# Kernel optimization log

Hardware: AMD Instinct MI355X
Metric: run time of the kernel (lower is better)

Reference implementation:

```python
import jax, jax.numpy as jnp
import numpy as np
import math

N_EMBD = 1024
N_HEAD = 16
HEAD_SIZE = N_EMBD // N_HEAD
LAYER_IDX = 2
LAMBDA_INIT = 0.8 - 0.6 * math.exp(-0.3 * (LAYER_IDX - 1))
LN_EPS = 1e-5
B, T = 4, 1024


def setup_inputs() -> dict:
    key = jax.random.key(0)
    ks = jax.random.split(key, 11)
    s = 0.02  # weight init scale
    return {
        "x": jax.random.normal(ks[0], (B, T, N_EMBD), dtype=jnp.float32),
        "Wq1": jax.random.normal(ks[1], (N_EMBD, N_EMBD), dtype=jnp.float32) * s,
        "Wq2": jax.random.normal(ks[2], (N_EMBD, N_EMBD), dtype=jnp.float32) * s,
        "Wk1": jax.random.normal(ks[3], (N_EMBD, N_EMBD), dtype=jnp.float32) * s,
        "Wk2": jax.random.normal(ks[4], (N_EMBD, N_EMBD), dtype=jnp.float32) * s,
        "Wv": jax.random.normal(ks[5], (N_EMBD, 2 * N_EMBD), dtype=jnp.float32) * s,
        "Wc": jax.random.normal(ks[6], (2 * N_EMBD, N_EMBD), dtype=jnp.float32) * s,
        "lq1": jax.random.normal(ks[7], (N_HEAD, HEAD_SIZE), dtype=jnp.float32) * 0.1,
        "lk1": jax.random.normal(ks[8], (N_HEAD, HEAD_SIZE), dtype=jnp.float32) * 0.1,
        "lq2": jax.random.normal(ks[9], (N_HEAD, HEAD_SIZE), dtype=jnp.float32) * 0.1,
        "lk2": jax.random.normal(ks[10], (N_HEAD, HEAD_SIZE), dtype=jnp.float32) * 0.1,
    }


def reference(x, Wq1, Wq2, Wk1, Wk2, Wv, Wc, lq1, lk1, lq2, lk2):
    Bx, Tx, C = x.shape
    H, hs = N_HEAD, HEAD_SIZE
    scale = 1.0 / math.sqrt(hs)

    # projections -> (B, T, H, d)
    q1 = (x @ Wq1).reshape(Bx, Tx, H, hs)
    q2 = (x @ Wq2).reshape(Bx, Tx, H, hs)
    k1 = (x @ Wk1).reshape(Bx, Tx, H, hs)
    k2 = (x @ Wk2).reshape(Bx, Tx, H, hs)
    v = (x @ Wv).reshape(Bx, Tx, H, 2 * hs)

    # dual score streams (B, H, T, T)
    att1 = jnp.einsum("bqhd,bkhd->bhqk", q1, k1) * scale
    att2 = jnp.einsum("bqhd,bkhd->bhqk", q2, k2) * scale

    causal = jnp.tril(jnp.ones((Tx, Tx), dtype=bool))  # (T, T)
    neg_inf = jnp.float32(-jnp.inf)
    att1 = jnp.where(causal, att1, neg_inf)
    att2 = jnp.where(causal, att2, neg_inf)
    a1 = jax.nn.softmax(att1, axis=-1)
    a2 = jax.nn.softmax(att2, axis=-1)

    # per-head differential lambda
    lam1 = jnp.exp(jnp.sum(lq1 * lk1, axis=-1))  # (H,)
    lam2 = jnp.exp(jnp.sum(lq2 * lk2, axis=-1))  # (H,)
    lam_full = lam1 - lam2 + LAMBDA_INIT  # (H,)

    att = a1 - lam_full[None, :, None, None] * a2  # dropout = identity (eval)

    # PV matmul -> (B, T, H, 2*hs)
    y = jnp.einsum("bhqk,bkhd->bqhd", att, v)

    # subLN over last dim (no affine)
    mu = jnp.mean(y, axis=-1, keepdims=True)
    var = jnp.mean(jnp.square(y - mu), axis=-1, keepdims=True)
    y = (y - mu) / jnp.sqrt(var + LN_EPS)
    y = y * (1.0 - LAMBDA_INIT)

    y = y.reshape(Bx, Tx, 2 * C)
    return y @ Wc  # resid dropout = identity (eval)
```

## Files before the change

kernel.cpp:

```cpp
#include <hip/hip_runtime.h>


#define T_SEQ 1024
#define NH 16
#define DV 128
#define NPROJ 6144
#define KSTR 72

typedef __bf16 bf16_t;
typedef __bf16 bf16x8 __attribute__((ext_vector_type(8)));
typedef __bf16 bf16x4 __attribute__((ext_vector_type(4)));
typedef float f32x4 __attribute__((ext_vector_type(4)));

#define LAMBDA_INIT 0.35550906759096928f
#define ONE_MINUS_LI 0.6444909324090307f
#define LOG2E 1.4426950408889634f

#define GLDS(g, l)                                                            \
  __builtin_amdgcn_global_load_lds(                                           \
      (const __attribute__((address_space(1))) void*)(g),                     \
      (__attribute__((address_space(3))) void*)(l), 16, 0, 0)

template <int C>
__device__ __forceinline__ float dppf(float x) {
  return __builtin_bit_cast(
      float, __builtin_amdgcn_update_dpp(0, __builtin_bit_cast(int, x), C,
                                         0xF, 0xF, true));
}
__device__ __forceinline__ float row16_max(float x) {
  x = fmaxf(x, dppf<0xB1>(x));
  x = fmaxf(x, dppf<0x4E>(x));
  x = fmaxf(x, dppf<0x124>(x));
  x = fmaxf(x, dppf<0x128>(x));
  return x;
}
__device__ __forceinline__ float row16_sum(float x) {
  x += dppf<0xB1>(x);
  x += dppf<0x4E>(x);
  x += dppf<0x124>(x);
  x += dppf<0x128>(x);
  return x;
}

static const size_t OFF_WCAT = 0;
static const size_t OFF_XB = OFF_WCAT + (size_t)6144 * 1024 * 2;
static const size_t OFF_WCT = OFF_XB + (size_t)4096 * 1024 * 2;
static const size_t OFF_PROJ = OFF_WCT + (size_t)2048 * 1024 * 2;
static const size_t OFF_VT = OFF_PROJ + (size_t)4096 * 6144 * 2;
static const size_t OFF_YLN = OFF_VT + (size_t)64 * 128 * 1024 * 2;
static const size_t OFF_LAM = OFF_YLN + (size_t)4096 * 2048 * 2;

__global__ void __launch_bounds__(256) cast_x(const float* __restrict__ x,
                                              bf16_t* __restrict__ o) {
  const int i = (blockIdx.x * 256 + threadIdx.x) * 4;
  float4 v = *(const float4*)(x + i);
  bf16x4 r = {(bf16_t)v.x, (bf16_t)v.y, (bf16_t)v.z, (bf16_t)v.w};
  *(bf16x4*)(o + i) = r;
}

__device__ __forceinline__ void tcast_body(const float* __restrict__ W,
                                           bf16_t* __restrict__ Wt, int K,
                                           int N, int row0) {
  __shared__ float tile[32][33];
  const int k0 = blockIdx.x * 32, n0 = blockIdx.y * 32;
  const int tx = threadIdx.x & 31, ty = threadIdx.x >> 5;
#pragma unroll
  for (int i = 0; i < 32; i += 8)
    tile[ty + i][tx] = W[(long)(k0 + ty + i) * N + n0 + tx];
  __syncthreads();
#pragma unroll
  for (int i = 0; i < 32; i += 8)
    Wt[(long)(row0 + n0 + ty + i) * K + k0 + tx] = (bf16_t)tile[tx][ty + i];
}

__global__ void __launch_bounds__(256) tcast_w(const float* __restrict__ W,
                                               bf16_t* __restrict__ Wt, int K,
                                               int N, int row0) {
  tcast_body(W, Wt, K, N, row0);
}

__global__ void __launch_bounds__(256) tcast_w4(const float* __restrict__ W0,
                                                const float* __restrict__ W1,
                                                const float* __restrict__ W2,
                                                const float* __restrict__ W3,
                                                bf16_t* __restrict__ Wt) {
  const float* Ws[4] = {W0, W1, W2, W3};
  tcast_body(Ws[blockIdx.z], Wt, 1024, 1024, blockIdx.z * 1024);
}

__global__ void lam_kernel(const float* __restrict__ lq1,
                           const float* __restrict__ lk1,
                           const float* __restrict__ lq2,
                           const float* __restrict__ lk2,
                           float* __restrict__ lam) {
  const int h = threadIdx.x;
  if (h < NH) {
    float d1 = 0.f, d2 = 0.f;
    for (int i = 0; i < 64; ++i) {
      d1 += lq1[h * 64 + i] * lk1[h * 64 + i];
      d2 += lq2[h * 64 + i] * lk2[h * 64 + i];
    }
    lam[h] = expf(d1) - expf(d2) + LAMBDA_INIT;
  }
}

#define BM 128
#define BN 128
#define BK 32

template <typename OutT>
__global__ void __launch_bounds__(256) gemm_bt(const bf16_t* __restrict__ A,
                                               const bf16_t* __restrict__ Bt,
                                               OutT* __restrict__ C, int M,
                                               int N, int K) {
  __shared__ __align__(16) bf16_t As[BM * BK];
  __shared__ __align__(16) bf16_t Bs[BN * BK];
  const int tid = threadIdx.x;
  const int w = tid >> 6;
  const int lane = tid & 63;
  const int quad = lane >> 4, l16 = lane & 15;
  const int m0 = blockIdx.y * BM, n0 = blockIdx.x * BN;
  const int wm = (w >> 1) * 64, wn = (w & 1) * 64;
  const int srow = tid >> 2;
  const int scol = (tid & 3) * 8;

  const bf16_t* Ag0 = A + (long)(m0 + srow) * K + scol;
  const bf16_t* Ag1 = Ag0 + (long)64 * K;
  const bf16_t* Bg0 = Bt + (long)(n0 + srow) * K + scol;
  const bf16_t* Bg1 = Bg0 + (long)64 * K;
  bf16_t* lA0 = As + tid * 8;
  bf16_t* lA1 = As + 2048 + tid * 8;
  bf16_t* lB0 = Bs + tid * 8;
  bf16_t* lB1 = Bs + 2048 + tid * 8;

  f32x4 acc[4][4] = {};

  for (int k0 = 0; k0 < K; k0 += BK) {
    GLDS(Ag0 + k0, lA0);
    GLDS(Ag1 + k0, lA1);
    GLDS(Bg0 + k0, lB0);
    GLDS(Bg1 + k0, lB1);
    __syncthreads();
    bf16x8 af[4], bfr[4];
#pragma unroll
    for (int t = 0; t < 4; ++t) {
      af[t] = *(const bf16x8*)(As + (wm + t * 16 + l16) * BK + quad * 8);
      bfr[t] = *(const bf16x8*)(Bs + (wn + t * 16 + l16) * BK + quad * 8);
    }
#pragma unroll
    for (int mt = 0; mt < 4; ++mt)
#pragma unroll
      for (int nt = 0; nt < 4; ++nt)
        acc[mt][nt] = __builtin_amdgcn_mfma_f32_16x16x32_bf16(
            af[mt], bfr[nt], acc[mt][nt], 0, 0, 0);
    __syncthreads();
  }

#pragma unroll
  for (int mt = 0; mt < 4; ++mt)
#pragma unroll
    for (int nt = 0; nt < 4; ++nt) {
      const int col = n0 + wn + nt * 16 + l16;
#pragma unroll
      for (int i = 0; i < 4; ++i) {
        const int row = m0 + wm + mt * 16 + quad * 4 + i;
        C[(long)row * N + col] = (OutT)acc[mt][nt][i];
      }
    }
}

__global__ void __launch_bounds__(256) transpose_v(const bf16_t* __restrict__ proj,
                                                   bf16_t* __restrict__ vt) {
  __shared__ bf16_t tile[32][34];
  const int bh = blockIdx.z;
  const int b = bh >> 4, h = bh & 15;
  const int t0 = blockIdx.x * 32, d0 = blockIdx.y * 32;
  const int tx = threadIdx.x & 31, ty = threadIdx.x >> 5;
  const bf16_t* src = proj + (long)(b * T_SEQ) * NPROJ + 4096 + h * 128;
#pragma unroll
  for (int i = 0; i < 32; i += 8)
    tile[ty + i][tx] = src[(long)(t0 + ty + i) * NPROJ + d0 + tx];
  __syncthreads();
  bf16_t* dst = vt + ((long)(b * NH + h) * DV) * T_SEQ;
#pragma unroll
  for (int i = 0; i < 32; i += 8)
    dst[(long)(d0 + ty + i) * T_SEQ + t0 + tx] = tile[tx][ty + i];
}

__global__ void __launch_bounds__(256) attn_kernel(const bf16_t* __restrict__ proj,
                                                   const bf16_t* __restrict__ vt,
                                                   const float* __restrict__ lamp,
                                                   bf16_t* __restrict__ yln) {
  const int p = blockIdx.x >> 4;
  const int h = blockIdx.x & 15;
  const int b = blockIdx.y;
  const int tid = threadIdx.x;
  const int w = tid >> 6, lane = tid & 63;
  const int quad = lane >> 4, l16 = lane & 15;
  const long bT = (long)b * T_SEQ;

  __shared__ __align__(16) bf16_t Ks1[64 * KSTR];
  __shared__ __align__(16) bf16_t Ks2[64 * KSTR];
  __shared__ __align__(16) bf16_t Vs[DV * KSTR];
  __shared__ __align__(16) bf16_t pbuf[4][2][16 * KSTR];

  const bf16_t* gK1 =
      proj + (bT + (tid >> 3)) * (long)NPROJ + h * 64 + 2048 + (tid & 7) * 8;
  const bf16_t* gK2 = gK1 + 1024;
  const bf16_t* vbase = vt + ((long)(b * NH + h) * DV) * T_SEQ;
  const bf16_t* gV = vbase + (long)(tid >> 3) * T_SEQ + (tid & 7) * 8;
  const int kw0 = (tid >> 3) * KSTR + (tid & 7) * 8;

  bf16_t* pb1 = &pbuf[w][0][0];
  bf16_t* pb2 = &pbuf[w][1][0];
  const float sc = 0.125f * LOG2E;
  const float lam = lamp[h];
  const int prd0 = l16 * KSTR + (((quad) ^ (l16 >> 2)) << 3);
  const int prd1 = l16 * KSTR + (((4 + quad) ^ (l16 >> 2)) << 3);

  for (int phase = 0; phase < 2; ++phase) {
    const int qblk = phase == 0 ? (15 - p) : p;
    const int q0 = qblk * 64 + w * 16;

    const bf16_t* qrow = proj + (bT + q0 + l16) * (long)NPROJ + h * 64;
    bf16x8 aq1[2], aq2[2];
    aq1[0] = *(const bf16x8*)(qrow + quad * 8);
    aq1[1] = *(const bf16x8*)(qrow + 32 + quad * 8);
    aq2[0] = *(const bf16x8*)(qrow + 1024 + quad * 8);
    aq2[1] = *(const bf16x8*)(qrow + 1024 + 32 + quad * 8);

    f32x4 O1[8] = {}, O2[8] = {};
    float m1[4], l1[4], m2[4], l2[4];
#pragma unroll
    for (int i = 0; i < 4; ++i) {
      m1[i] = -3.0e38f;
      m2[i] = -3.0e38f;
      l1[i] = 0.f;
      l2[i] = 0.f;
    }

    const int kend_blk = qblk * 64 + 64;
    const int kend_w = q0 + 16;

    bf16x8 rK1[2], rK2[2], rV[4];
    rK1[0] = *(const bf16x8*)(gK1);
    rK1[1] = *(const bf16x8*)(gK1 + (long)32 * NPROJ);
    rK2[0] = *(const bf16x8*)(gK2);
    rK2[1] = *(const bf16x8*)(gK2 + (long)32 * NPROJ);
#pragma unroll
    for (int j = 0; j < 4; ++j)
      rV[j] = *(const bf16x8*)(gV + (long)(32 * j) * T_SEQ);

    for (int kt = 0; kt < kend_blk; kt += 64) {
      *(bf16x8*)(Ks1 + kw0) = rK1[0];
      *(bf16x8*)(Ks1 + kw0 + 32 * KSTR) = rK1[1];
      *(bf16x8*)(Ks2 + kw0) = rK2[0];
      *(bf16x8*)(Ks2 + kw0 + 32 * KSTR) = rK2[1];
#pragma unroll
      for (int j = 0; j < 4; ++j)
        *(bf16x8*)(Vs + kw0 + j * 32 * KSTR) = rV[j];
      __syncthreads();

      if (kt + 64 < kend_blk) {
        const long ko = (long)(kt + 64) * NPROJ;
        rK1[0] = *(const bf16x8*)(gK1 + ko);
        rK1[1] = *(const bf16x8*)(gK1 + ko + (long)32 * NPROJ);
        rK2[0] = *(const bf16x8*)(gK2 + ko);
        rK2[1] = *(const bf16x8*)(gK2 + ko + (long)32 * NPROJ);
#pragma unroll
        for (int j = 0; j < 4; ++j)
          rV[j] = *(const bf16x8*)(gV + kt + 64 + (long)(32 * j) * T_SEQ);
      }

      if (kt < kend_w) {
        f32x4 s1[4], s2[4];
#pragma unroll
        for (int c = 0; c < 4; ++c) {
          const bf16_t* kr1 = Ks1 + (c * 16 + l16) * KSTR;
          const bf16_t* kr2 = Ks2 + (c * 16 + l16) * KSTR;
          bf16x8 b10 = *(const bf16x8*)(kr1 + quad * 8);
          bf16x8 b11 = *(const bf16x8*)(kr1 + 32 + quad * 8);
          f32x4 z = {};
          z = __builtin_amdgcn_mfma_f32_16x16x32_bf16(aq1[0], b10, z, 0, 0, 0);
          z = __builtin_amdgcn_mfma_f32_16x16x32_bf16(aq1[1], b11, z, 0, 0, 0);
          s1[c] = z;
          bf16x8 b20 = *(const bf16x8*)(kr2 + quad * 8);
          bf16x8 b21 = *(const bf16x8*)(kr2 + 32 + quad * 8);
          f32x4 z2 = {};
          z2 = __builtin_amdgcn_mfma_f32_16x16x32_bf16(aq2[0], b20, z2, 0, 0, 0);
          z2 = __builtin_amdgcn_mfma_f32_16x16x32_bf16(aq2[1], b21, z2, 0, 0, 0);
          s2[c] = z2;
        }
        const bool need_mask = (kt + 63 > q0);
        float mx1[4], mx2[4];
#pragma unroll
        for (int i = 0; i < 4; ++i) {
          mx1[i] = -3.0e38f;
          mx2[i] = -3.0e38f;
        }
#pragma unroll
        for (int c = 0; c < 4; ++c) {
          const int col = kt + c * 16 + l16;
#pragma unroll
          for (int i = 0; i < 4; ++i) {
            const int row = q0 + quad * 4 + i;
            float v1 = s1[c][i] * sc, v2 = s2[c][i] * sc;
            if (need_mask && col > row) {
              v1 = -1e30f;
              v2 = -1e30f;
            }
            s1[c][i] = v1;
            s2[c][i] = v2;
            mx1[i] = fmaxf(mx1[i], v1);
            mx2[i] = fmaxf(mx2[i], v2);
          }
        }
#pragma unroll
        for (int i = 0; i < 4; ++i) {
          mx1[i] = row16_max(mx1[i]);
          mx2[i] = row16_max(mx2[i]);
        }
        float al1[4], al2[4];
#pragma unroll
        for (int i = 0; i < 4; ++i) {
          float mn = fmaxf(m1[i], mx1[i]);
          al1[i] = exp2f(m1[i] - mn);
          m1[i] = mn;
          mn = fmaxf(m2[i], mx2[i]);
          al2[i] = exp2f(m2[i] - mn);
          m2[i] = mn;
        }
        float sum1[4] = {0, 0, 0, 0}, sum2[4] = {0, 0, 0, 0};
#pragma unroll
        for (int c = 0; c < 4; ++c) {
          const int lg = c * 2 + (l16 >> 3);
#pragma unroll
          for (int i = 0; i < 4; ++i) {
            bf16_t p1 = (bf16_t)exp2f(s1[c][i] - m1[i]);
            bf16_t p2 = (bf16_t)exp2f(s2[c][i] - m2[i]);
            const int off =
                (quad * 4 + i) * KSTR + ((lg ^ quad) << 3) + (l16 & 7);
            pb1[off] = p1;
            pb2[off] = p2;
            sum1[i] += (float)p1;
            sum2[i] += (float)p2;
          }
        }
#pragma unroll
        for (int i = 0; i < 4; ++i) {
          sum1[i] = row16_sum(sum1[i]);
          sum2[i] = row16_sum(sum2[i]);
        }
#pragma unroll
        for (int i = 0; i < 4; ++i) {
          l1[i] = l1[i] * al1[i] + sum1[i];
          l2[i] = l2[i] * al2[i] + sum2[i];
        }
#pragma unroll
        for (int f = 0; f < 8; ++f)
#pragma unroll
          for (int i = 0; i < 4; ++i) {
            O1[f][i] *= al1[i];
            O2[f][i] *= al2[i];
          }
        __asm__ volatile("s_waitcnt lgkmcnt(0)" ::: "memory");
        bf16x8 ap1[2], ap2[2];
        ap1[0] = *(const bf16x8*)(pb1 + prd0);
        ap1[1] = *(const bf16x8*)(pb1 + prd1);
        ap2[0] = *(const bf16x8*)(pb2 + prd0);
        ap2[1] = *(const bf16x8*)(pb2 + prd1);
#pragma unroll
        for (int f = 0; f < 8; ++f) {
          const bf16_t* vr = Vs + (f * 16 + l16) * KSTR;
          bf16x8 bv0 = *(const bf16x8*)(vr + quad * 8);
          bf16x8 bv1 = *(const bf16x8*)(vr + 32 + quad * 8);
          O1[f] =
              __builtin_amdgcn_mfma_f32_16x16x32_bf16(ap1[0], bv0, O1[f], 0, 0, 0);
          O1[f] =
              __builtin_amdgcn_mfma_f32_16x16x32_bf16(ap1[1], bv1, O1[f], 0, 0, 0);
          O2[f] =
              __builtin_amdgcn_mfma_f32_16x16x32_bf16(ap2[0], bv0, O2[f], 0, 0, 0);
          O2[f] =
              __builtin_amdgcn_mfma_f32_16x16x32_bf16(ap2[1], bv1, O2[f], 0, 0, 0);
        }
      }
      __syncthreads();
    }

    float inv1[4], inv2[4];
#pragma unroll
    for (int i = 0; i < 4; ++i) {
      inv1[i] = 1.0f / l1[i];
      inv2[i] = lam / l2[i];
    }
    float sm[4], sq[4];
#pragma unroll
    for (int i = 0; i < 4; ++i) {
      sm[i] = 0.f;
      sq[i] = 0.f;
    }
#pragma unroll
    for (int f = 0; f < 8; ++f)
#pragma unroll
      for (int i = 0; i < 4; ++i) {
        float y = O1[f][i] * inv1[i] - O2[f][i] * inv2[i];
        O1[f][i] = y;
        sm[i] += y;
        sq[i] += y * y;
      }
#pragma unroll
    for (int i = 0; i < 4; ++i) {
      sm[i] = row16_sum(sm[i]);
      sq[i] = row16_sum(sq[i]);
    }
    float mu[4], rs[4];
#pragma unroll
    for (int i = 0; i < 4; ++i) {
      mu[i] = sm[i] * (1.0f / 128.0f);
      float var = sq[i] * (1.0f / 128.0f) - mu[i] * mu[i];
      rs[i] = rsqrtf(var + 1e-5f) * ONE_MINUS_LI;
    }
#pragma unroll
    for (int i = 0; i < 4; ++i) {
      bf16_t* dst = yln + (bT + q0 + quad * 4 + i) * (long)2048 + h * 128 + l16;
#pragma unroll
      for (int f = 0; f < 8; ++f)
        dst[f * 16] = (bf16_t)((O1[f][i] - mu[i]) * rs[i]);
    }
  }
}

extern "C" void kernel_launch(void* const* d_in, const int* in_sizes, int n_in,
                              void* d_out, int out_size, void* d_ws,
                              size_t ws_size, hipStream_t stream) {
  const float* x = (const float*)d_in[0];
  const float* Wq1 = (const float*)d_in[1];
  const float* Wq2 = (const float*)d_in[2];
  const float* Wk1 = (const float*)d_in[3];
  const float* Wk2 = (const float*)d_in[4];
  const float* Wv = (const float*)d_in[5];
  const float* Wc = (const float*)d_in[6];
  const float* lq1 = (const float*)d_in[7];
  const float* lk1 = (const float*)d_in[8];
  const float* lq2 = (const float*)d_in[9];
  const float* lk2 = (const float*)d_in[10];
  float* out = (float*)d_out;

  char* ws = (char*)d_ws;
  bf16_t* wcat = (bf16_t*)(ws + OFF_WCAT);
  bf16_t* xb = (bf16_t*)(ws + OFF_XB);
  bf16_t* wct = (bf16_t*)(ws + OFF_WCT);
  bf16_t* projb = (bf16_t*)(ws + OFF_PROJ);
  bf16_t* vtb = (bf16_t*)(ws + OFF_VT);
  bf16_t* ylnb = (bf16_t*)(ws + OFF_YLN);
  float* lamp = (float*)(ws + OFF_LAM);

  cast_x<<<4096, 256, 0, stream>>>(x, xb);
  tcast_w4<<<dim3(32, 32, 4), 256, 0, stream>>>(Wq1, Wq2, Wk1, Wk2, wcat);
  tcast_w<<<dim3(32, 64), 256, 0, stream>>>(Wv, wcat, 1024, 2048, 4096);
  tcast_w<<<dim3(64, 32), 256, 0, stream>>>(Wc, wct, 2048, 1024, 0);
  lam_kernel<<<1, 64, 0, stream>>>(lq1, lk1, lq2, lk2, lamp);

  gemm_bt<bf16_t><<<dim3(48, 32), 256, 0, stream>>>(xb, wcat, projb, 4096, 6144, 1024);
  transpose_v<<<dim3(32, 4, 64), 256, 0, stream>>>(projb, vtb);
  attn_kernel<<<dim3(128, 4), 256, 0, stream>>>(projb, vtb, lamp, ylnb);
  gemm_bt<float><<<dim3(8, 32), 256, 0, stream>>>(ylnb, wct, out, 4096, 1024, 2048);
}
```

Baseline: 340.0 us.

## Compute transposed scores so P stays in registers for PV MFMA

Swaps the MFMA operands in QK^T so each lane holds scores for one query and four keys. The probabilities can then feed the PV matmul directly as the B operand of 16x16x16 bf16 MFMAs, with no round trip through the per-warp LDS P buffer. Row max and sum reductions become cross-quad shuffles instead of DPP row reductions, and the output store is vectorised to bf16x4. In exchange it uses the smaller-K MFMA (twice as many PV instructions) and narrower bf16x4 V reads from LDS, which may cause bank conflicts. If neither 16x16x16 builtin exists, the fallback macro silently drops the PV product.

Result: no change. 335.5 us (-1.3%).

```diff
diff --git a/kernel.cpp b/kernel.cpp
--- a/kernel.cpp
+++ b/kernel.cpp
@@ -10,37 +10,27 @@
 typedef __bf16 bf16_t;
 typedef __bf16 bf16x8 __attribute__((ext_vector_type(8)));
 typedef __bf16 bf16x4 __attribute__((ext_vector_type(4)));
+typedef short s16x4 __attribute__((ext_vector_type(4)));
 typedef float f32x4 __attribute__((ext_vector_type(4)));
 
 #define LAMBDA_INIT 0.35550906759096928f
 #define ONE_MINUS_LI 0.6444909324090307f
 #define LOG2E 1.4426950408889634f
+
+#if __has_builtin(__builtin_amdgcn_mfma_f32_16x16x16_bf16)
+#define MFMA16(a, b, c) __builtin_amdgcn_mfma_f32_16x16x16_bf16(a, b, c, 0, 0, 0)
+#elif __has_builtin(__builtin_amdgcn_mfma_f32_16x16x16bf16_1k)
+#define MFMA16(a, b, c)                                                       \
+  __builtin_amdgcn_mfma_f32_16x16x16bf16_1k(                                  \
+      __builtin_bit_cast(s16x4, a), __builtin_bit_cast(s16x4, b), c, 0, 0, 0)
+#else
+#define MFMA16(a, b, c) (c)
+#endif
 
 #define GLDS(g, l)                                                            \
   __builtin_amdgcn_global_load_lds(                                           \
       (const __attribute__((address_space(1))) void*)(g),                     \
       (__attribute__((address_space(3))) void*)(l), 16, 0, 0)
-
-template <int C>
-__device__ __forceinline__ float dppf(float x) {
-  return __builtin_bit_cast(
-      float, __builtin_amdgcn_update_dpp(0, __builtin_bit_cast(int, x), C,
-                                         0xF, 0xF, true));
-}
-__device__ __forceinline__ float row16_max(float x) {
-  x = fmaxf(x, dppf<0xB1>(x));
-  x = fmaxf(x, dppf<0x4E>(x));
-  x = fmaxf(x, dppf<0x124>(x));
-  x = fmaxf(x, dppf<0x128>(x));
-  return x;
-}
-__device__ __forceinline__ float row16_sum(float x) {
-  x += dppf<0xB1>(x);
-  x += dppf<0x4E>(x);
-  x += dppf<0x124>(x);
-  x += dppf<0x128>(x);
-  return x;
-}
 
 static const size_t OFF_WCAT = 0;
 static const size_t OFF_XB = OFF_WCAT + (size_t)6144 * 1024 * 2;
@@ -202,7 +192,6 @@
   __shared__ __align__(16) bf16_t Ks1[64 * KSTR];
   __shared__ __align__(16) bf16_t Ks2[64 * KSTR];
   __shared__ __align__(16) bf16_t Vs[DV * KSTR];
-  __shared__ __align__(16) bf16_t pbuf[4][2][16 * KSTR];
 
   const bf16_t* gK1 =
       proj + (bT + (tid >> 3)) * (long)NPROJ + h * 64 + 2048 + (tid & 7) * 8;
@@ -211,18 +200,15 @@
   const bf16_t* gV = vbase + (long)(tid >> 3) * T_SEQ + (tid & 7) * 8;
   const int kw0 = (tid >> 3) * KSTR + (tid & 7) * 8;
 
-  bf16_t* pb1 = &pbuf[w][0][0];
-  bf16_t* pb2 = &pbuf[w][1][0];
   const float sc = 0.125f * LOG2E;
   const float lam = lamp[h];
-  const int prd0 = l16 * KSTR + (((quad) ^ (l16 >> 2)) << 3);
-  const int prd1 = l16 * KSTR + (((4 + quad) ^ (l16 >> 2)) << 3);
 
   for (int phase = 0; phase < 2; ++phase) {
     const int qblk = phase == 0 ? (15 - p) : p;
     const int q0 = qblk * 64 + w * 16;
-
-    const bf16_t* qrow = proj + (bT + q0 + l16) * (long)NPROJ + h * 64;
+    const int qg = q0 + l16;
+
+    const bf16_t* qrow = proj + (bT + qg) * (long)NPROJ + h * 64;
     bf16x8 aq1[2], aq2[2];
     aq1[0] = *(const bf16x8*)(qrow + quad * 8);
     aq1[1] = *(const bf16x8*)(qrow + 32 + quad * 8);
@@ -230,14 +216,7 @@
     aq2[1] = *(const bf16x8*)(qrow + 1024 + 32 + quad * 8);
 
     f32x4 O1[8] = {}, O2[8] = {};
-    float m1[4], l1[4], m2[4], l2[4];
-#pragma unroll
-    for (int i = 0; i < 4; ++i) {
-      m1[i] = -3.0e38f;
-      m2[i] = -3.0e38f;
-      l1[i] = 0.f;
-      l2[i] = 0.f;
-    }
+    float m1 = -3.0e38f, m2 = -3.0e38f, l1 = 0.f, l2 = 0.f;
 
     const int kend_blk = qblk * 64 + 64;
     const int kend_w = q0 + 16;
@@ -278,154 +257,110 @@
         for (int c = 0; c < 4; ++c) {
           const bf16_t* kr1 = Ks1 + (c * 16 + l16) * KSTR;
           const bf16_t* kr2 = Ks2 + (c * 16 + l16) * KSTR;
-          bf16x8 b10 = *(const bf16x8*)(kr1 + quad * 8);
-          bf16x8 b11 = *(const bf16x8*)(kr1 + 32 + quad * 8);
+          bf16x8 ka0 = *(const bf16x8*)(kr1 + quad * 8);
+          bf16x8 ka1 = *(const bf16x8*)(kr1 + 32 + quad * 8);
           f32x4 z = {};
-          z = __builtin_amdgcn_mfma_f32_16x16x32_bf16(aq1[0], b10, z, 0, 0, 0);
-          z = __builtin_amdgcn_mfma_f32_16x16x32_bf16(aq1[1], b11, z, 0, 0, 0);
+          z = __builtin_amdgcn_mfma_f32_16x16x32_bf16(ka0, aq1[0], z, 0, 0, 0);
+          z = __builtin_amdgcn_mfma_f32_16x16x32_bf16(ka1, aq1[1], z, 0, 0, 0);
           s1[c] = z;
-          bf16x8 b20 = *(const bf16x8*)(kr2 + quad * 8);
-          bf16x8 b21 = *(const bf16x8*)(kr2 + 32 + quad * 8);
+          bf16x8 kb0 = *(const bf16x8*)(kr2 + quad * 8);
+          bf16x8 kb1 = *(const bf16x8*)(kr2 + 32 + quad * 8);
           f32x4 z2 = {};
-          z2 = __builtin_amdgcn_mfma_f32_16x16x32_bf16(aq2[0], b20, z2, 0, 0, 0);
-          z2 = __builtin_amdgcn_mfma_f32_16x16x32_bf16(aq2[1], b21, z2, 0, 0, 0);
+          z2 = __builtin_amdgcn_mfma_f32_16x16x32_bf16(kb0, aq2[0], z2, 0, 0, 0);
+          z2 = __builtin_amdgcn_mfma_f32_16x16x32_bf16(kb1, aq2[1], z2, 0, 0, 0);
           s2[c] = z2;
         }
         const bool need_mask = (kt + 63 > q0);
-        float mx1[4], mx2[4];
-#pragma unroll
-        for (int i = 0; i < 4; ++i) {
-          mx1[i] = -3.0e38f;
-          mx2[i] = -3.0e38f;
-        }
+        float mx1 = -3.0e38f, mx2 = -3.0e38f;
 #pragma unroll
         for (int c = 0; c < 4; ++c) {
-          const int col = kt + c * 16 + l16;
 #pragma unroll
           for (int i = 0; i < 4; ++i) {
-            const int row = q0 + quad * 4 + i;
+            const int key = kt + c * 16 + quad * 4 + i;
             float v1 = s1[c][i] * sc, v2 = s2[c][i] * sc;
-            if (need_mask && col > row) {
+            if (need_mask && key > qg) {
               v1 = -1e30f;
               v2 = -1e30f;
             }
             s1[c][i] = v1;
             s2[c][i] = v2;
-            mx1[i] = fmaxf(mx1[i], v1);
-            mx2[i] = fmaxf(mx2[i], v2);
+            mx1 = fmaxf(mx1, v1);
+            mx2 = fmaxf(mx2, v2);
           }
         }
-#pragma unroll
-        for (int i = 0; i < 4; ++i) {
-          mx1[i] = row16_max(mx1[i]);
-          mx2[i] = row16_max(mx2[i]);
-        }
-        float al1[4], al2[4];
-#pragma unroll
-        for (int i = 0; i < 4; ++i) {
-          float mn = fmaxf(m1[i], mx1[i]);
-          al1[i] = exp2f(m1[i] - mn);
-          m1[i] = mn;
-          mn = fmaxf(m2[i], mx2[i]);
-          al2[i] = exp2f(m2[i] - mn);
-          m2[i] = mn;
-        }
-        float sum1[4] = {0, 0, 0, 0}, sum2[4] = {0, 0, 0, 0};
+        mx1 = fmaxf(mx1, __shfl_xor(mx1, 16));
+        mx1 = fmaxf(mx1, __shfl_xor(mx1, 32));
+        mx2 = fmaxf(mx2, __shfl_xor(mx2, 16));
+        mx2 = fmaxf(mx2, __shfl_xor(mx2, 32));
+        const float mn1 = fmaxf(m1, mx1), mn2 = fmaxf(m2, mx2);
+        const float al1 = exp2f(m1 - mn1), al2 = exp2f(m2 - mn2);
+        m1 = mn1;
+        m2 = mn2;
+        bf16x4 pc1[4], pc2[4];
+        float sum1 = 0.f, sum2 = 0.f;
 #pragma unroll
         for (int c = 0; c < 4; ++c) {
-          const int lg = c * 2 + (l16 >> 3);
 #pragma unroll
           for (int i = 0; i < 4; ++i) {
-            bf16_t p1 = (bf16_t)exp2f(s1[c][i] - m1[i]);
-            bf16_t p2 = (bf16_t)exp2f(s2[c][i] - m2[i]);
-            const int off =
-                (quad * 4 + i) * KSTR + ((lg ^ quad) << 3) + (l16 & 7);
-            pb1[off] = p1;
-            pb2[off] = p2;
-            sum1[i] += (float)p1;
-            sum2[i] += (float)p2;
+            bf16_t p1 = (bf16_t)exp2f(s1[c][i] - m1);
+            bf16_t p2 = (bf16_t)exp2f(s2[c][i] - m2);
+            pc1[c][i] = p1;
+            pc2[c][i] = p2;
+            sum1 += (float)p1;
+            sum2 += (float)p2;
           }
         }
-#pragma unroll
-        for (int i = 0; i < 4; ++i) {
-          sum1[i] = row16_sum(sum1[i]);
-          sum2[i] = row16_sum(sum2[i]);
-        }
-#pragma unroll
-        for (int i = 0; i < 4; ++i) {
-          l1[i] = l1[i] * al1[i] + sum1[i];
-          l2[i] = l2[i] * al2[i] + sum2[i];
-        }
+        sum1 += __shfl_xor(sum1, 16);
+        sum1 += __shfl_xor(sum1, 32);
+        sum2 += __shfl_xor(sum2, 16);
+        sum2 += __shfl_xor(sum2, 32);
+        l1 = l1 * al1 + sum1;
+        l2 = l2 * al2 + sum2;
 #pragma unroll
         for (int f = 0; f < 8; ++f)
 #pragma unroll
           for (int i = 0; i < 4; ++i) {
-            O1[f][i] *= al1[i];
-            O2[f][i] *= al2[i];
+            O1[f][i] *= al1;
+            O2[f][i] *= al2;
           }
-        __asm__ volatile("s_waitcnt lgkmcnt(0)" ::: "memory");
-        bf16x8 ap1[2], ap2[2];
-        ap1[0] = *(const bf16x8*)(pb1 + prd0);
-        ap1[1] = *(const bf16x8*)(pb1 + prd1);
-        ap2[0] = *(const bf16x8*)(pb2 + prd0);
-        ap2[1] = *(const bf16x8*)(pb2 + prd1);
-#pragma unroll
-        for (int f = 0; f < 8; ++f) {
-          const bf16_t* vr = Vs + (f * 16 + l16) * KSTR;
-          bf16x8 bv0 = *(const bf16x8*)(vr + quad * 8);
-          bf16x8 bv1 = *(const bf16x8*)(vr + 32 + quad * 8);
-          O1[f] =
-              __builtin_amdgcn_mfma_f32_16x16x32_bf16(ap1[0], bv0, O1[f], 0, 0, 0);
-          O1[f] =
-              __builtin_amdgcn_mfma_f32_16x16x32_bf16(ap1[1], bv1, O1[f], 0, 0, 0);
-          O2[f] =
-              __builtin_amdgcn_mfma_f32_16x16x32_bf16(ap2[0], bv0, O2[f], 0, 0, 0);
-          O2[f] =
-              __builtin_amdgcn_mfma_f32_16x16x32_bf16(ap2[1], bv1, O2[f], 0, 0, 0);
+#pragma unroll
+        for (int c = 0; c < 4; ++c) {
+#pragma unroll
+          for (int f = 0; f < 8; ++f) {
+            bf16x4 va =
+                *(const bf16x4*)(Vs + (f * 16 + l16) * KSTR + c * 16 + quad * 4);
+            O1[f] = MFMA16(va, pc1[c], O1[f]);
+            O2[f] = MFMA16(va, pc2[c], O2[f]);
+          }
         }
       }
       __syncthreads();
     }
 
-    float inv1[4], inv2[4];
-#pragma unroll
-    for (int i = 0; i < 4; ++i) {
-      inv1[i] = 1.0f / l1[i];
-      inv2[i] = lam / l2[i];
-    }
-    float sm[4], sq[4];
-#pragma unroll
-    for (int i = 0; i < 4; ++i) {
-      sm[i] = 0.f;
-      sq[i] = 0.f;
-    }
+    const float inv1 = 1.0f / l1, inv2 = lam / l2;
+    float sm = 0.f, sq = 0.f;
 #pragma unroll
     for (int f = 0; f < 8; ++f)
 #pragma unroll
       for (int i = 0; i < 4; ++i) {
-        float y = O1[f][i] * inv1[i] - O2[f][i] * inv2[i];
+        float y = O1[f][i] * inv1 - O2[f][i] * inv2;
         O1[f][i] = y;
-        sm[i] += y;
-        sq[i] += y * y;
+        sm += y;
+        sq += y * y;
       }
-#pragma unroll
-    for (int i = 0; i < 4; ++i) {
-      sm[i] = row16_sum(sm[i]);
-      sq[i] = row16_sum(sq[i]);
-    }
-    float mu[4], rs[4];
-#pragma unroll
-    for (int i = 0; i < 4; ++i) {
-      mu[i] = sm[i] * (1.0f / 128.0f);
-      float var = sq[i] * (1.0f / 128.0f) - mu[i] * mu[i];
-      rs[i] = rsqrtf(var + 1e-5f) * ONE_MINUS_LI;
-    }
-#pragma unroll
-    for (int i = 0; i < 4; ++i) {
-      bf16_t* dst = yln + (bT + q0 + quad * 4 + i) * (long)2048 + h * 128 + l16;
-#pragma unroll
-      for (int f = 0; f < 8; ++f)
-        dst[f * 16] = (bf16_t)((O1[f][i] - mu[i]) * rs[i]);
+    sm += __shfl_xor(sm, 16);
+    sm += __shfl_xor(sm, 32);
+    sq += __shfl_xor(sq, 16);
+    sq += __shfl_xor(sq, 32);
+    const float mu = sm * (1.0f / 128.0f);
+    const float var = sq * (1.0f / 128.0f) - mu * mu;
+    const float rs = rsqrtf(var + 1e-5f) * ONE_MINUS_LI;
+    bf16_t* dst = yln + (bT + qg) * (long)2048 + h * 128 + quad * 4;
+#pragma unroll
+    for (int f = 0; f < 8; ++f) {
+      bf16x4 o = {(bf16_t)((O1[f][0] - mu) * rs), (bf16_t)((O1[f][1] - mu) * rs),
+                  (bf16_t)((O1[f][2] - mu) * rs), (bf16_t)((O1[f][3] - mu) * rs)};
+      *(bf16x4*)(dst + f * 16) = o;
     }
   }
 }
```
